# Optimization experiments

Hardware: AMD Instinct MI355X
Metric: run time of the kernel (lower is better)

Reference implementation:

```python
import jax, jax.numpy as jnp
import numpy as np

U2 = 1024          # unit2
DIM = 3 * U2       # input_dim == units == 3072
BATCH = 16384


def _build_mask(rng: np.random.Generator) -> np.ndarray:
    """Reconstruct the STN block-structured binary mask, shape (units, input_dim).

    Row blocks (units) x col blocks (inputs), each U2 x U2:
      rows [0,U2):      [ones,        Bern(1/2), zeros     ]
      rows [U2,2U2):    [Bern(1/2),   Bern(3/4), Bern(1/2) ]
      rows [2U2,3U2):   [zeros,       Bern(1/2), ones      ]
    """
    def bern(p, shape):
        return (rng.random(shape) < p).astype(np.float32)
    ones = np.ones((U2, U2), np.float32)
    zeros = np.zeros((U2, U2), np.float32)
    row1 = np.concatenate([ones, bern(0.5, (U2, U2)), zeros], axis=1)
    row2 = np.concatenate([bern(0.5, (U2, U2)), bern(0.75, (U2, U2)), bern(0.5, (U2, U2))], axis=1)
    row3 = np.concatenate([zeros, bern(0.5, (U2, U2)), ones], axis=1)
    return np.concatenate([row1, row2, row3], axis=0)


def setup_inputs() -> dict:
    key = jax.random.key(0)
    kx, kw = jax.random.split(key)
    x = jax.random.normal(kx, (BATCH, DIM), dtype=jnp.float32)
    # w init: uniform [0, 0.01], non-negative constraint holds at init
    w = jax.random.uniform(kw, (DIM, DIM), dtype=jnp.float32, minval=0.0, maxval=0.01)
    b = jnp.zeros((DIM,), dtype=jnp.float32)  # stn_bias = [0, 0]
    mask = jnp.asarray(_build_mask(np.random.default_rng(0)))
    return {"x": x, "w": w, "b": b, "mask": mask}


def reference(x, w, b, mask):
    # Original: p = transpose(s @ x^T) -> (B, units, dim); f = diag_part(p @ w) + b
    # Algebraic identity: f[b,u] = b[u] + sum_d mask[u,d] * x[b,d] * w[d,u]
    # i.e. a dense matmul against the masked weight W_eff[d,u] = mask[u,d] * w[d,u].
    w_eff = mask.T * w                     # (dim, units)
    return x @ w_eff + b                   # (batch, units)
```

## Files before the change

kernel.cpp:

```cpp
#include <hip/hip_runtime.h>
#include <hip/hip_bf16.h>
#include <stdint.h>

#define DIM   3072
#define BATCH 16384

typedef __attribute__((ext_vector_type(8))) short bf16x8;
typedef __attribute__((ext_vector_type(4))) float f32x4;

__device__ __forceinline__ unsigned short f2b(float f) {
    union { float f; unsigned u; } c; c.f = f;
    unsigned u = c.u;
    unsigned r = (u + 0x7fffu + ((u >> 16) & 1u)) >> 16;
    return (unsigned short)r;
}

__global__ void cvt_x_kernel(const float* __restrict__ x, ushort* __restrict__ xb, int n4) {
    int stride = gridDim.x * blockDim.x;
    for (int i = blockIdx.x * blockDim.x + threadIdx.x; i < n4; i += stride) {
        float4 v = reinterpret_cast<const float4*>(x)[i];
        ushort4 o;
        o.x = f2b(v.x); o.y = f2b(v.y); o.z = f2b(v.z); o.w = f2b(v.w);
        reinterpret_cast<ushort4*>(xb)[i] = o;
    }
}

__global__ void build_wt_kernel(const float* __restrict__ w, const float* __restrict__ mask,
                                ushort* __restrict__ wt) {
    __shared__ float tile[64][65];
    const int u0 = blockIdx.x * 64;
    const int d0 = blockIdx.y * 64;
    const int t  = threadIdx.x;
    const int rr = t >> 4, cc = t & 15;
#pragma unroll
    for (int it = 0; it < 4; ++it) {
        int drow = it * 16 + rr;
        float4 v = *reinterpret_cast<const float4*>(&w[(size_t)(d0 + drow) * DIM + u0 + cc * 4]);
        tile[drow][cc * 4 + 0] = v.x;
        tile[drow][cc * 4 + 1] = v.y;
        tile[drow][cc * 4 + 2] = v.z;
        tile[drow][cc * 4 + 3] = v.w;
    }
    __syncthreads();
#pragma unroll
    for (int it = 0; it < 4; ++it) {
        int urow = it * 16 + rr;
        float4 mv = *reinterpret_cast<const float4*>(&mask[(size_t)(u0 + urow) * DIM + d0 + cc * 4]);
        ushort4 o;
        o.x = f2b(tile[cc * 4 + 0][urow] * mv.x);
        o.y = f2b(tile[cc * 4 + 1][urow] * mv.y);
        o.z = f2b(tile[cc * 4 + 2][urow] * mv.z);
        o.w = f2b(tile[cc * 4 + 3][urow] * mv.w);
        *reinterpret_cast<ushort4*>(&wt[(size_t)(u0 + urow) * DIM + d0 + cc * 4]) = o;
    }
}

#define GLOAD_LDS16(g, l)                                                                 \
    __builtin_amdgcn_global_load_lds((const __attribute__((address_space(1))) void*)(g),  \
                                     (__attribute__((address_space(3))) void*)(l), 16, 0, 0)

__global__ __launch_bounds__(256) void gemm_f32_kernel(const float* __restrict__ Af,
                                                       const ushort* __restrict__ Bt,
                                                       const float* __restrict__ bias,
                                                       float* __restrict__ C) {
    constexpr int BK = 32;
    __shared__ ushort As[128 * BK];
    __shared__ ushort Bs[128 * BK];
    const int tid  = threadIdx.x;
    const int lane = tid & 63;
    const int wid  = tid >> 6;
    const int wr = wid >> 1, wc = wid & 1;
    const int brow = blockIdx.y * 128;
    const int bcol = blockIdx.x * 128;
    const int r16 = lane & 15, kg = lane >> 4;
    f32x4 acc[4][4] = {};
    for (int k0 = 0; k0 < DIM; k0 += BK) {
#pragma unroll
        for (int p = 0; p < 4; ++p) {
            int row = p * 32 + (tid >> 3);
            int f4  = tid & 7;
            float4 v = *reinterpret_cast<const float4*>(
                &Af[(size_t)(brow + row) * DIM + k0 + f4 * 4]);
            ushort4 o; o.x = f2b(v.x); o.y = f2b(v.y); o.z = f2b(v.z); o.w = f2b(v.w);
            *reinterpret_cast<ushort4*>(&As[row * BK + f4 * 4]) = o;
        }
#pragma unroll
        for (int c = 0; c < 2; ++c) {
            int q = wid * 2 + c;
            int row = q * 16 + (lane >> 2);
            const ushort* gp = Bt + (size_t)(bcol + row) * DIM + k0 + (lane & 3) * 8;
            GLOAD_LDS16(gp, Bs + q * 512);
        }
        __syncthreads();
        bf16x8 a[4], b[4];
#pragma unroll
        for (int i = 0; i < 4; ++i)
            a[i] = *reinterpret_cast<const bf16x8*>(&As[(wr * 64 + i * 16 + r16) * BK + kg * 8]);
#pragma unroll
        for (int j = 0; j < 4; ++j)
            b[j] = *reinterpret_cast<const bf16x8*>(&Bs[(wc * 64 + j * 16 + r16) * BK + kg * 8]);
#pragma unroll
        for (int i = 0; i < 4; ++i)
#pragma unroll
            for (int j = 0; j < 4; ++j)
                acc[i][j] = __builtin_amdgcn_mfma_f32_16x16x32_bf16(a[i], b[j], acc[i][j], 0, 0, 0);
        __syncthreads();
    }
#pragma unroll
    for (int j = 0; j < 4; ++j) {
        int col = bcol + wc * 64 + j * 16 + r16;
        float bv = bias[col];
#pragma unroll
        for (int i = 0; i < 4; ++i) {
            int row0 = brow + wr * 64 + i * 16 + kg * 4;
#pragma unroll
            for (int r = 0; r < 4; ++r)
                C[(size_t)(row0 + r) * DIM + col] = acc[i][j][r] + bv;
        }
    }
}

__global__ __launch_bounds__(512, 1) void gemm8p(const ushort* __restrict__ A,
                                                 const ushort* __restrict__ B,
                                                 const float* __restrict__ bias,
                                                 float* __restrict__ C) {
    __shared__ ushort sh[2 * 2 * 16384];

    const int tid  = threadIdx.x;
    const int lane = tid & 63;
    const int wid  = tid >> 6;
    const int wr   = wid >> 2;
    const int wc   = wid & 3;
    const int l15  = lane & 15;
    const int kg   = lane >> 4;
    const int sx   = lane & 7;

    const int srow = lane >> 3;
    const int sg   = (lane & 7) ^ srow;

    const int orig = blockIdx.x;
    const int wg   = (orig & 7) * (gridDim.x >> 3) + (orig >> 3);
    const int tm   = wg / 12;
    const int tn   = wg - tm * 12;
    const int brow = tm * 256, bcol = tn * 256;

    f32x4 acc[8][4] = {};
    bf16x8 a_[8], b0_[4], b1_[4];

#define STAGE(b, side, h, tt)                                                              \
    do {                                                                                   \
        int _t = (tt) < 47 ? (tt) : 47;                                                    \
        const ushort* _base = (side) ? B : A;                                              \
        int _r0 = ((side) ? bcol : brow) + (h) * 128 + wid * 16 + srow;                    \
        const ushort* _g0 = _base + (size_t)_r0 * DIM + _t * 64 + sg * 8;                  \
        ushort* _l0 = sh + ((b) * 2 + (side)) * 16384 + (h) * 8192 + wid * 1024;           \
        GLOAD_LDS16(_g0, _l0);                                                             \
        GLOAD_LDS16(_g0 + (size_t)8 * DIM, _l0 + 512);                                     \
    } while (0)

#define LDA(QB, QM)                                                                        \
    _Pragma("unroll") for (int fm = 0; fm < 4; ++fm)                                       \
    _Pragma("unroll") for (int ks = 0; ks < 2; ++ks)                                       \
        a_[fm * 2 + ks] = *reinterpret_cast<const bf16x8*>(                                \
            sh + (QB) * 32768 + (wr * 128 + (QM) * 64 + fm * 16 + l15) * 64 +              \
            (((ks * 4 + kg) ^ sx) * 8));

#define LDB(DST, QB, QN)                                                                   \
    _Pragma("unroll") for (int fn = 0; fn < 2; ++fn)                                       \
    _Pragma("unroll") for (int ks = 0; ks < 2; ++ks)                                       \
        DST[fn * 2 + ks] = *reinterpret_cast<const bf16x8*>(                               \
            sh + (QB) * 32768 + 16384 + (wc * 64 + (QN) * 32 + fn * 16 + l15) * 64 +       \
            (((ks * 4 + kg) ^ sx) * 8));

#define MMQ(QM, QN, BARR)                                                                  \
    _Pragma("unroll") for (int fm = 0; fm < 4; ++fm)                                       \
    _Pragma("unroll") for (int fn = 0; fn < 2; ++fn)                                       \
    _Pragma("unroll") for (int ks = 0; ks < 2; ++ks)                                       \
        acc[(QM) * 4 + fm][(QN) * 2 + fn] = __builtin_amdgcn_mfma_f32_16x16x32_bf16(       \
            a_[fm * 2 + ks], BARR[fn * 2 + ks], acc[(QM) * 4 + fm][(QN) * 2 + fn], 0, 0, 0);

#define MIDSYNC()                                                                          \
    __builtin_amdgcn_s_barrier();                                                          \
    asm volatile("s_waitcnt lgkmcnt(0)" ::: "memory");                                     \
    __builtin_amdgcn_sched_barrier(0);                                                     \
    __builtin_amdgcn_s_setprio(1);

#define ENDPHASE()                                                                         \
    __builtin_amdgcn_s_setprio(0);                                                         \
    __builtin_amdgcn_s_barrier();

    STAGE(0, 0, 0, 0);
    STAGE(0, 0, 1, 0);
    STAGE(0, 1, 0, 0);
    STAGE(0, 1, 1, 0);
    STAGE(1, 1, 0, 1);
    STAGE(1, 1, 1, 1);
    asm volatile("s_waitcnt vmcnt(4)" ::: "memory");
    __builtin_amdgcn_s_barrier();

    for (int t = 0; t < 48; t += 2) {
        LDA(0, 0); LDB(b0_, 0, 0);
        STAGE(1, 0, 0, t + 1);
        MIDSYNC(); MMQ(0, 0, b0_); ENDPHASE();
        LDB(b1_, 0, 1);
        STAGE(1, 0, 1, t + 1);
        MIDSYNC(); MMQ(0, 1, b1_); ENDPHASE();
        LDA(0, 1);
        STAGE(0, 1, 0, t + 2);
        MIDSYNC(); MMQ(1, 0, b0_); ENDPHASE();
        STAGE(0, 1, 1, t + 2);
        asm volatile("s_waitcnt vmcnt(4)" ::: "memory");
        MIDSYNC(); MMQ(1, 1, b1_); ENDPHASE();
        LDA(1, 0); LDB(b0_, 1, 0);
        STAGE(0, 0, 0, t + 2);
        MIDSYNC(); MMQ(0, 0, b0_); ENDPHASE();
        LDB(b1_, 1, 1);
        STAGE(0, 0, 1, t + 2);
        MIDSYNC(); MMQ(0, 1, b1_); ENDPHASE();
        LDA(1, 1);
        STAGE(1, 1, 0, t + 3);
        MIDSYNC(); MMQ(1, 0, b0_); ENDPHASE();
        STAGE(1, 1, 1, t + 3);
        asm volatile("s_waitcnt vmcnt(4)" ::: "memory");
        MIDSYNC(); MMQ(1, 1, b1_); ENDPHASE();
    }

#pragma unroll
    for (int n = 0; n < 4; ++n) {
        int col = bcol + wc * 64 + n * 16 + l15;
        float bv = bias[col];
#pragma unroll
        for (int m = 0; m < 8; ++m) {
            int row0 = brow + wr * 128 + m * 16 + kg * 4;
#pragma unroll
            for (int r = 0; r < 4; ++r)
                C[(size_t)(row0 + r) * DIM + col] = acc[m][n][r] + bv;
        }
    }
#undef STAGE
#undef LDA
#undef LDB
#undef MMQ
#undef MIDSYNC
#undef ENDPHASE
}

extern "C" void kernel_launch(void* const* d_in, const int* in_sizes, int n_in,
                              void* d_out, int out_size, void* d_ws, size_t ws_size,
                              hipStream_t stream) {
    const float* x    = (const float*)d_in[0];
    const float* w    = (const float*)d_in[1];
    const float* bias = (const float*)d_in[2];
    const float* mask = (const float*)d_in[3];
    float* out = (float*)d_out;

    const size_t wt_bytes = (size_t)DIM * DIM * sizeof(ushort);
    const size_t xb_off   = (wt_bytes + 255) & ~(size_t)255;
    const size_t xb_bytes = (size_t)BATCH * DIM * sizeof(ushort);

    ushort* wt = (ushort*)d_ws;
    ushort* xb = (ushort*)((char*)d_ws + xb_off);

    build_wt_kernel<<<dim3(DIM / 64, DIM / 64), 256, 0, stream>>>(w, mask, wt);

    if (ws_size >= xb_off + xb_bytes) {
        cvt_x_kernel<<<2048, 256, 0, stream>>>(x, xb, BATCH * DIM / 4);
        gemm8p<<<(BATCH / 256) * (DIM / 256), 512, 0, stream>>>(xb, wt, bias, out);
    } else {
        gemm_f32_kernel<<<dim3(DIM / 128, BATCH / 128), 256, 0, stream>>>(x, wt, bias, out);
    }
}
```

Measured before the change: 350.4 us.

## Fuse fp32-to-bf16 conversion of X into GEMM A-tile staging

Drops the separate cvt_x pass that wrote a bf16 copy of X. The GEMM now loads fp32 X into registers, converts to bf16 in-kernel, and writes the swizzled tile to LDS. The pipeline schedule is reworked so that A register loads and LDS writes interleave with the B direct-to-LDS loads and the MFMA phases. This removes one full read and write of the 16384x3072 activation. In exchange, the GEMM reads fp32 X (twice the bytes per tile), uses more VGPRs for staging, and adds conversion ALU work inside the main loop.

```diff
diff --git a/kernel.cpp b/kernel.cpp
--- a/kernel.cpp
+++ b/kernel.cpp
@@ -15,14 +15,11 @@
     return (unsigned short)r;
 }
 
-__global__ void cvt_x_kernel(const float* __restrict__ x, ushort* __restrict__ xb, int n4) {
-    int stride = gridDim.x * blockDim.x;
-    for (int i = blockIdx.x * blockDim.x + threadIdx.x; i < n4; i += stride) {
-        float4 v = reinterpret_cast<const float4*>(x)[i];
-        ushort4 o;
-        o.x = f2b(v.x); o.y = f2b(v.y); o.z = f2b(v.z); o.w = f2b(v.w);
-        reinterpret_cast<ushort4*>(xb)[i] = o;
-    }
+__device__ __forceinline__ bf16x8 cvt8(float4 a, float4 b) {
+    union { unsigned short h[8]; bf16x8 v; } u;
+    u.h[0] = f2b(a.x); u.h[1] = f2b(a.y); u.h[2] = f2b(a.z); u.h[3] = f2b(a.w);
+    u.h[4] = f2b(b.x); u.h[5] = f2b(b.y); u.h[6] = f2b(b.z); u.h[7] = f2b(b.w);
+    return u.v;
 }
 
 __global__ void build_wt_kernel(const float* __restrict__ w, const float* __restrict__ mask,
@@ -120,7 +117,7 @@
     }
 }
 
-__global__ __launch_bounds__(512, 1) void gemm8p(const ushort* __restrict__ A,
+__global__ __launch_bounds__(512, 1) void gemm8p(const float* __restrict__ X,
                                                  const ushort* __restrict__ B,
                                                  const float* __restrict__ bias,
                                                  float* __restrict__ C) {
@@ -146,16 +143,36 @@
 
     f32x4 acc[8][4] = {};
     bf16x8 a_[8], b0_[4], b1_[4];
-
-#define STAGE(b, side, h, tt)                                                              \
+    float4 a0v[4], a1v[4];
+
+#define BSTAGE(b, h, tt)                                                                   \
     do {                                                                                   \
         int _t = (tt) < 47 ? (tt) : 47;                                                    \
-        const ushort* _base = (side) ? B : A;                                              \
-        int _r0 = ((side) ? bcol : brow) + (h) * 128 + wid * 16 + srow;                    \
-        const ushort* _g0 = _base + (size_t)_r0 * DIM + _t * 64 + sg * 8;                  \
-        ushort* _l0 = sh + ((b) * 2 + (side)) * 16384 + (h) * 8192 + wid * 1024;           \
+        int _r0 = bcol + (h) * 128 + wid * 16 + srow;                                      \
+        const ushort* _g0 = B + (size_t)_r0 * DIM + _t * 64 + sg * 8;                      \
+        ushort* _l0 = sh + ((b) * 2 + 1) * 16384 + (h) * 8192 + wid * 1024;                \
         GLOAD_LDS16(_g0, _l0);                                                             \
         GLOAD_LDS16(_g0 + (size_t)8 * DIM, _l0 + 512);                                     \
+    } while (0)
+
+#define ALOAD(dst, h, tt)                                                                  \
+    do {                                                                                   \
+        int _t = (tt) < 47 ? (tt) : 47;                                                    \
+        int _r0 = brow + (h) * 128 + wid * 16 + srow;                                      \
+        const float* _g = X + (size_t)_r0 * DIM + _t * 64 + sg * 8;                        \
+        dst[0] = *reinterpret_cast<const float4*>(_g);                                     \
+        dst[1] = *reinterpret_cast<const float4*>(_g + 4);                                 \
+        dst[2] = *reinterpret_cast<const float4*>(_g + (size_t)8 * DIM);                   \
+        dst[3] = *reinterpret_cast<const float4*>(_g + (size_t)8 * DIM + 4);               \
+    } while (0)
+
+#define AWRITE(src, b, h)                                                                  \
+    do {                                                                                   \
+        bf16x8 _w0 = cvt8(src[0], src[1]);                                                 \
+        bf16x8 _w1 = cvt8(src[2], src[3]);                                                 \
+        ushort* _l = sh + (b) * 32768 + (h) * 8192 + wid * 1024 + srow * 64 + (lane & 7) * 8; \
+        *reinterpret_cast<bf16x8*>(_l) = _w0;                                              \
+        *reinterpret_cast<bf16x8*>(_l + 512) = _w1;                                        \
     } while (0)
 
 #define LDA(QB, QM)                                                                        \
@@ -189,39 +206,47 @@
     __builtin_amdgcn_s_setprio(0);                                                         \
     __builtin_amdgcn_s_barrier();
 
-    STAGE(0, 0, 0, 0);
-    STAGE(0, 0, 1, 0);
-    STAGE(0, 1, 0, 0);
-    STAGE(0, 1, 1, 0);
-    STAGE(1, 1, 0, 1);
-    STAGE(1, 1, 1, 1);
-    asm volatile("s_waitcnt vmcnt(4)" ::: "memory");
+    ALOAD(a0v, 0, 0);
+    ALOAD(a1v, 1, 0);
+    BSTAGE(0, 0, 0);
+    BSTAGE(0, 1, 0);
+    BSTAGE(1, 0, 1);
+    BSTAGE(1, 1, 1);
+    AWRITE(a0v, 0, 0);
+    AWRITE(a1v, 0, 1);
+    asm volatile("s_waitcnt vmcnt(4) lgkmcnt(0)" ::: "memory");
     __builtin_amdgcn_s_barrier();
 
     for (int t = 0; t < 48; t += 2) {
         LDA(0, 0); LDB(b0_, 0, 0);
-        STAGE(1, 0, 0, t + 1);
+        ALOAD(a0v, 0, t + 1);
         MIDSYNC(); MMQ(0, 0, b0_); ENDPHASE();
         LDB(b1_, 0, 1);
-        STAGE(1, 0, 1, t + 1);
+        ALOAD(a1v, 1, t + 1);
         MIDSYNC(); MMQ(0, 1, b1_); ENDPHASE();
         LDA(0, 1);
-        STAGE(0, 1, 0, t + 2);
+        BSTAGE(0, 0, t + 2);
+        asm volatile("s_waitcnt vmcnt(6)" ::: "memory");
+        AWRITE(a0v, 1, 0);
         MIDSYNC(); MMQ(1, 0, b0_); ENDPHASE();
-        STAGE(0, 1, 1, t + 2);
+        BSTAGE(0, 1, t + 2);
         asm volatile("s_waitcnt vmcnt(4)" ::: "memory");
+        AWRITE(a1v, 1, 1);
         MIDSYNC(); MMQ(1, 1, b1_); ENDPHASE();
         LDA(1, 0); LDB(b0_, 1, 0);
-        STAGE(0, 0, 0, t + 2);
+        ALOAD(a0v, 0, t + 2);
         MIDSYNC(); MMQ(0, 0, b0_); ENDPHASE();
         LDB(b1_, 1, 1);
-        STAGE(0, 0, 1, t + 2);
+        ALOAD(a1v, 1, t + 2);
         MIDSYNC(); MMQ(0, 1, b1_); ENDPHASE();
         LDA(1, 1);
-        STAGE(1, 1, 0, t + 3);
+        BSTAGE(1, 0, t + 3);
+        asm volatile("s_waitcnt vmcnt(6)" ::: "memory");
+        AWRITE(a0v, 0, 0);
         MIDSYNC(); MMQ(1, 0, b0_); ENDPHASE();
-        STAGE(1, 1, 1, t + 3);
+        BSTAGE(1, 1, t + 3);
         asm volatile("s_waitcnt vmcnt(4)" ::: "memory");
+        AWRITE(a1v, 0, 1);
         MIDSYNC(); MMQ(1, 1, b1_); ENDPHASE();
     }
 
@@ -237,7 +262,9 @@
                 C[(size_t)(row0 + r) * DIM + col] = acc[m][n][r] + bv;
         }
     }
-#undef STAGE
+#undef BSTAGE
+#undef ALOAD
+#undef AWRITE
 #undef LDA
 #undef LDB
 #undef MMQ
@@ -254,19 +281,8 @@
     const float* mask = (const float*)d_in[3];
     float* out = (float*)d_out;
 
-    const size_t wt_bytes = (size_t)DIM * DIM * sizeof(ushort);
-    const size_t xb_off   = (wt_bytes + 255) & ~(size_t)255;
-    const size_t xb_bytes = (size_t)BATCH * DIM * sizeof(ushort);
-
     ushort* wt = (ushort*)d_ws;
-    ushort* xb = (ushort*)((char*)d_ws + xb_off);
 
     build_wt_kernel<<<dim3(DIM / 64, DIM / 64), 256, 0, stream>>>(w, mask, wt);
-
-    if (ws_size >= xb_off + xb_bytes) {
-        cvt_x_kernel<<<2048, 256, 0, stream>>>(x, xb, BATCH * DIM / 4);
-        gemm8p<<<(BATCH / 256) * (DIM / 256), 512, 0, stream>>>(xb, wt, bias, out);
-    } else {
-        gemm_f32_kernel<<<dim3(DIM / 128, BATCH / 128), 256, 0, stream>>>(x, wt, bias, out);
-    }
-}
+    gemm8p<<<(BATCH / 256) * (DIM / 256), 512, 0, stream>>>(x, wt, bias, out);
+}
```

Measured after the change: 604.0 us. 72.3% more time.
